# Kernel tuning notes

Hardware: AMD Instinct MI355X
Metric: run time of the kernel (lower is better)

Reference implementation:

```python
import jax, jax.numpy as jnp
import numpy as np

B, N, E = 8, 1024, 512
H, D = 8, 64
F = 2048


def setup_inputs() -> dict:
    key = jax.random.key(0)
    ks = jax.random.split(key, 12)
    s = lambda *sh: 1.0 / np.sqrt(sh[-1])
    inp = {
        "input1": jax.random.normal(ks[0], (B, N, E), dtype=jnp.float32),
        # projection weights stored as [in, out] (torch weight transposed)
        "Wq": jax.random.normal(ks[1], (E, H * D), dtype=jnp.float32) * s(E, E),
        "Wk": jax.random.normal(ks[2], (E, H * D), dtype=jnp.float32) * s(E, E),
        "Wv": jax.random.normal(ks[3], (E, H * D), dtype=jnp.float32) * s(E, E),
        "Wo": jax.random.normal(ks[4], (H * D, E), dtype=jnp.float32) * s(E, E),
        "bo": jnp.zeros((E,), dtype=jnp.float32),
        "g1": jnp.ones((E,), dtype=jnp.float32),
        "b1": jnp.zeros((E,), dtype=jnp.float32),
        "W1": jax.random.normal(ks[5], (E, F), dtype=jnp.float32) * s(E, E),
        "bf1": jnp.zeros((F,), dtype=jnp.float32),
        "W2": jax.random.normal(ks[6], (F, E), dtype=jnp.float32) * s(F, F),
        "bf2": jnp.zeros((E,), dtype=jnp.float32),
        "g2": jnp.ones((E,), dtype=jnp.float32),
        "b2": jnp.zeros((E,), dtype=jnp.float32),
    }
    return inp


def _layernorm(x, g, b, eps=1e-5):
    mu = jnp.mean(x, axis=-1, keepdims=True)
    var = jnp.var(x, axis=-1, keepdims=True)
    return (x - mu) * jax.lax.rsqrt(var + eps) * g + b


def reference(input1, Wq, Wk, Wv, Wo, bo, g1, b1, W1, bf1, W2, bf2, g2, b2):
    x = input1
    # QKV projections, split heads: [B, H, N, D]
    q = (x @ Wq).reshape(B, N, H, D).transpose(0, 2, 1, 3)
    k = (x @ Wk).reshape(B, N, H, D).transpose(0, 2, 1, 3)
    v = (x @ Wv).reshape(B, N, H, D).transpose(0, 2, 1, 3)
    # scaled dot-product attention (naive, materialized scores as in source)
    score = jnp.einsum("bhnd,bhmd->bhnm", q, k) / jnp.sqrt(jnp.float32(D))
    weights = jax.nn.softmax(score, axis=-1)
    out = jnp.einsum("bhnm,bhmd->bhnd", weights, v)
    out_concat = out.transpose(0, 2, 1, 3).reshape(B, N, H * D)
    mh = out_concat @ Wo + bo
    out1 = _layernorm(x + mh, g1, b1)
    ff = jax.nn.relu(out1 @ W1 + bf1) @ W2 + bf2
    out3 = _layernorm(out1 + ff, g2, b2)
    return (out3, 0)
```

## Files before the change

kernel.cpp:

```cpp
#include <hip/hip_runtime.h>
#include <cstdint>
#include <cstddef>

typedef _Float16 h8 __attribute__((ext_vector_type(8)));
typedef _Float16 h4 __attribute__((ext_vector_type(4)));
typedef __fp16   g2 __attribute__((ext_vector_type(2)));
typedef float    f32x4 __attribute__((ext_vector_type(4)));

constexpr int B_ = 8, N_ = 1024, E_ = 512, H_ = 8, D_ = 64, F_ = 2048;
constexpr int M_ = B_ * N_;
constexpr int HD_ = H_ * D_;

#define QSCALE2 0.18033688011112042f

#define GLOAD_LDS16(gp, lp)                                                        \
    __builtin_amdgcn_global_load_lds((const __attribute__((address_space(1))) void*)(gp), \
                                     (__attribute__((address_space(3))) void*)(lp), 16, 0, 0)

__device__ __forceinline__ float exp2_raw(float x) {
#if __has_builtin(__builtin_amdgcn_exp2f)
    return __builtin_amdgcn_exp2f(x);
#else
    float r;
    asm("v_exp_f32 %0, %1\n\ts_nop 0" : "=v"(r) : "v"(x));
    return r;
#endif
}

__global__ void __launch_bounds__(256) k_pre(
    const float* __restrict__ x, _Float16* __restrict__ xh,
    const float* __restrict__ Wq, const float* __restrict__ Wk,
    const float* __restrict__ Wv, const float* __restrict__ Wo,
    const float* __restrict__ W1, const float* __restrict__ W2,
    _Float16* __restrict__ oqkv, _Float16* __restrict__ oo,
    _Float16* __restrict__ o1, _Float16* __restrict__ o2) {
    if (blockIdx.z == 12) {
        int i = (blockIdx.x * 256 + threadIdx.x) * 16;
#pragma unroll
        for (int j = 0; j < 4; ++j) {
            float4 v = *(const float4*)(x + i + j * 4);
            h4 o = {(_Float16)v.x, (_Float16)v.y, (_Float16)v.z, (_Float16)v.w};
            *(h4*)(xh + i + j * 4) = o;
        }
        return;
    }
    if (blockIdx.x >= 256) return;
    const float* in;
    _Float16* out;
    int R, C, gt = blockIdx.x;
    switch (blockIdx.z) {
        case 0: in = Wq; out = oqkv;              R = 512;  C = 512;  break;
        case 1: in = Wk; out = oqkv + 512 * 512;  R = 512;  C = 512;  break;
        case 2: in = Wv; out = oqkv + 1024 * 512; R = 512;  C = 512;  break;
        case 3: in = Wo; out = oo;                R = 512;  C = 512;  break;
        default:
            if (blockIdx.z < 8) { in = W1; out = o1; R = 512;  C = 2048; gt += (blockIdx.z - 4) * 256; }
            else                { in = W2; out = o2; R = 2048; C = 512;  gt += (blockIdx.z - 8) * 256; }
    }
    const int ctiles = C >> 5;
    const int ty = gt / ctiles, tx = gt - ty * ctiles;
    const int r0 = ty * 32, c0 = tx * 32;
    __shared__ float lt[32][33];
    const int rr = threadIdx.x >> 3, cq = threadIdx.x & 7;
    float4 v = *(const float4*)&in[(size_t)(r0 + rr) * C + c0 + cq * 4];
    lt[rr][cq * 4 + 0] = v.x; lt[rr][cq * 4 + 1] = v.y;
    lt[rr][cq * 4 + 2] = v.z; lt[rr][cq * 4 + 3] = v.w;
    __syncthreads();
    h4 o = {(_Float16)lt[cq * 4 + 0][rr], (_Float16)lt[cq * 4 + 1][rr],
            (_Float16)lt[cq * 4 + 2][rr], (_Float16)lt[cq * 4 + 3][rr]};
    *(h4*)&out[(size_t)(c0 + rr) * R + r0 + cq * 4] = o;
}

template <int EPI>
__global__ void __launch_bounds__(256) k_gemm(
    const _Float16* __restrict__ A, const _Float16* __restrict__ Bt,
    int Mg, int Ng, int Kg,
    const float* __restrict__ bias,
    _Float16* __restrict__ outh,
    _Float16* __restrict__ qp, _Float16* __restrict__ kp, _Float16* __restrict__ vtp) {
    constexpr int BN = 128;
    constexpr int WN = BN / 2;
    constexpr int NI = WN / 16;
    __shared__ alignas(16) _Float16 lA[2][64 * 64];
    __shared__ alignas(16) _Float16 lB[2][BN * 64];

    const int tid = threadIdx.x;
    const int lane = tid & 63;
    const int wid = tid >> 6;
    const int wr = wid >> 1, wc = wid & 1;
    const int r16 = lane & 15, hseg = lane >> 4;

    const int bid = blockIdx.x;
    const int xcd = bid & 7;
    const int rem = bid >> 3;
    const int tx = rem >> 4, tyl = rem & 15;
    const int m0 = (xcd * 16 + tyl) * 64;
    const int n0 = tx * BN;

    auto STAGE = [&](int buf, int k0) {
#pragma unroll
        for (int i = 0; i < 2; ++i) {
            const int slot = i * 256 + tid, row = slot >> 3;
            const int cs = (slot & 7) ^ (row & 7);
            GLOAD_LDS16(A + (size_t)(m0 + row) * Kg + k0 + cs * 8, &lA[buf][slot * 8]);
        }
#pragma unroll
        for (int i = 0; i < BN / 32; ++i) {
            const int slot = i * 256 + tid, row = slot >> 3;
            const int cs = (slot & 7) ^ (row & 7);
            GLOAD_LDS16(Bt + (size_t)(n0 + row) * Kg + k0 + cs * 8, &lB[buf][slot * 8]);
        }
    };

    f32x4 acc[2][NI] = {};
    const int nt = Kg >> 6;

    STAGE(0, 0);
    __syncthreads();

    for (int t = 0; t < nt; ++t) {
        const int cur = t & 1;
        if (t + 1 < nt) STAGE(cur ^ 1, (t + 1) << 6);

#pragma unroll
        for (int kk = 0; kk < 2; ++kk) {
            h8 af[2], bf[NI];
#pragma unroll
            for (int mi = 0; mi < 2; ++mi) {
                const int row = wr * 32 + mi * 16 + r16;
                af[mi] = *(const h8*)&lA[cur][row * 64 + (((kk * 4 + hseg) ^ (row & 7)) * 8)];
            }
#pragma unroll
            for (int ni = 0; ni < NI; ++ni) {
                const int row = wc * WN + ni * 16 + r16;
                bf[ni] = *(const h8*)&lB[cur][row * 64 + (((kk * 4 + hseg) ^ (row & 7)) * 8)];
            }
#pragma unroll
            for (int mi = 0; mi < 2; ++mi)
#pragma unroll
                for (int ni = 0; ni < NI; ++ni)
                    acc[mi][ni] =
                        __builtin_amdgcn_mfma_f32_16x16x32_f16(af[mi], bf[ni], acc[mi][ni], 0, 0, 0);
        }
        __syncthreads();
    }

    if constexpr (EPI == 0) {
        if (n0 >= 1024) {
            _Float16* lC = &lA[0][0];
#pragma unroll
            for (int mi = 0; mi < 2; ++mi) {
                const int r0 = wr * 32 + mi * 16 + hseg * 4;
                const int s = r0 >> 3, ro = r0 & 7;
#pragma unroll
                for (int ni = 0; ni < NI; ++ni) {
                    const int c = wc * WN + ni * 16 + r16;
                    h4 pv = {(_Float16)acc[mi][ni][0], (_Float16)acc[mi][ni][1],
                             (_Float16)acc[mi][ni][2], (_Float16)acc[mi][ni][3]};
                    *(h4*)&lC[c * 64 + ((s ^ (c & 7)) << 3) + ro] = pv;
                }
            }
            __syncthreads();
            const int c = tid >> 1, half = tid & 1;
            const int b = m0 >> 10, nn0 = m0 & 1023;
            _Float16* gdst =
                vtp + ((size_t)(b * 512 + (n0 - 1024) + c)) * 1024 + nn0 + half * 32;
#pragma unroll
            for (int j = 0; j < 4; ++j) {
                const int s = half * 4 + j;
                h8 v = *(const h8*)&lC[c * 64 + ((s ^ (c & 7)) << 3)];
                *(h8*)&gdst[j * 8] = v;
            }
        } else {
#pragma unroll
            for (int mi = 0; mi < 2; ++mi)
#pragma unroll
                for (int ni = 0; ni < NI; ++ni)
#pragma unroll
                    for (int r = 0; r < 4; ++r) {
                        int row = m0 + wr * 32 + mi * 16 + hseg * 4 + r;
                        int col = n0 + wc * WN + ni * 16 + r16;
                        float v = acc[mi][ni][r];
                        int cc = col & 511;
                        int h = cc >> 6, d = cc & 63;
                        int b = row >> 10, nn = row & 1023;
                        if (col < 512)
                            qp[((b * 8 + h) * 1024 + nn) * 64 + d] = (_Float16)(v * QSCALE2);
                        else
                            kp[((b * 8 + h) * 1024 + nn) * 64 + d] = (_Float16)v;
                    }
        }
    } else {
#pragma unroll
        for (int mi = 0; mi < 2; ++mi)
#pragma unroll
            for (int ni = 0; ni < NI; ++ni)
#pragma unroll
                for (int r = 0; r < 4; ++r) {
                    int row = m0 + wr * 32 + mi * 16 + hseg * 4 + r;
                    int col = n0 + wc * WN + ni * 16 + r16;
                    float v = acc[mi][ni][r] + bias[col];
                    v = v > 0.f ? v : 0.f;
                    outh[(size_t)row * Ng + col] = (_Float16)v;
                }
    }
}

__global__ void __launch_bounds__(512) k_gemm64(
    const _Float16* __restrict__ A, const _Float16* __restrict__ Bt,
    int Ng, int Kg,
    const float* __restrict__ bias,
    const _Float16* __restrict__ resh, _Float16* __restrict__ outh) {
    __shared__ alignas(16) _Float16 lA[2][128 * 64];
    __shared__ alignas(16) _Float16 lB[2][64 * 64];

    const int tid = threadIdx.x;
    const int lane = tid & 63;
    const int wid = tid >> 6;
    const int wr = wid >> 1;
    const int wc = wid & 1;
    const int r16 = lane & 15, hseg = lane >> 4;

    const int bid = blockIdx.x;
    const int xcd = bid & 7;
    const int rem = bid >> 3;
    const int tx = rem >> 3, tyl = rem & 7;
    const int m0 = (xcd * 8 + tyl) * 128;
    const int n0 = tx * 64;

    auto STAGE = [&](int buf, int k0) {
#pragma unroll
        for (int i = 0; i < 2; ++i) {
            const int slot = i * 512 + tid, row = slot >> 3;
            const int cs = (slot & 7) ^ (row & 7);
            GLOAD_LDS16(A + (size_t)(m0 + row) * Kg + k0 + cs * 8, &lA[buf][slot * 8]);
        }
        {
            const int slot = tid, row = slot >> 3;
            const int cs = (slot & 7) ^ (row & 7);
            GLOAD_LDS16(Bt + (size_t)(n0 + row) * Kg + k0 + cs * 8, &lB[buf][slot * 8]);
        }
    };

    f32x4 acc[2][2] = {};
    const int nt = Kg >> 6;

    STAGE(0, 0);
    __syncthreads();

    for (int t = 0; t < nt; ++t) {
        const int cur = t & 1;
        if (t + 1 < nt) STAGE(cur ^ 1, (t + 1) << 6);

#pragma unroll
        for (int kk = 0; kk < 2; ++kk) {
            h8 af[2], bf[2];
#pragma unroll
            for (int mi = 0; mi < 2; ++mi) {
                const int row = wr * 32 + mi * 16 + r16;
                af[mi] = *(const h8*)&lA[cur][row * 64 + (((kk * 4 + hseg) ^ (row & 7)) * 8)];
            }
#pragma unroll
            for (int ni = 0; ni < 2; ++ni) {
                const int row = wc * 32 + ni * 16 + r16;
                bf[ni] = *(const h8*)&lB[cur][row * 64 + (((kk * 4 + hseg) ^ (row & 7)) * 8)];
            }
#pragma unroll
            for (int mi = 0; mi < 2; ++mi)
#pragma unroll
                for (int ni = 0; ni < 2; ++ni)
                    acc[mi][ni] =
                        __builtin_amdgcn_mfma_f32_16x16x32_f16(af[mi], bf[ni], acc[mi][ni], 0, 0, 0);
        }
        __syncthreads();
    }

#pragma unroll
    for (int mi = 0; mi < 2; ++mi)
#pragma unroll
        for (int ni = 0; ni < 2; ++ni)
#pragma unroll
            for (int r = 0; r < 4; ++r) {
                int row = m0 + wr * 32 + mi * 16 + hseg * 4 + r;
                int col = n0 + wc * 32 + ni * 16 + r16;
                float v = acc[mi][ni][r] + bias[col] + (float)resh[(size_t)row * Ng + col];
                outh[(size_t)row * Ng + col] = (_Float16)v;
            }
}

__global__ void __launch_bounds__(512) k_attn(const _Float16* __restrict__ q,
                                              const _Float16* __restrict__ k,
                                              const _Float16* __restrict__ vt,
                                              _Float16* __restrict__ attn) {
    __shared__ alignas(16) _Float16 lK[2][64 * 64];
    __shared__ alignas(16) _Float16 lV[2][64 * 64];
    __shared__ alignas(16) _Float16 lP[8][16 * 64];

    const int tid = threadIdx.x, lane = tid & 63, w = tid >> 6;
    const int bid = blockIdx.x;
    const int xcd = bid & 7, rem = bid >> 3;
    const int bh = xcd * 8 + (rem & 7);
    const int q0 = (rem >> 3) * 128;
    const int r16 = lane & 15, hseg = lane >> 4;
    const size_t base = (size_t)bh * N_ * D_;

    h8 qf0 = *(const h8*)&q[base + (size_t)(q0 + w * 16 + r16) * 64 + hseg * 8];
    h8 qf1 = *(const h8*)&q[base + (size_t)(q0 + w * 16 + r16) * 64 + 32 + hseg * 8];

    const int srow = tid >> 3;
    const int scsrc = (tid & 7) ^ (srow & 7);

    auto STAGE = [&](int buf, int kt) {
        GLOAD_LDS16(k + base + kt * 4096 + srow * 64 + scsrc * 8, &lK[buf][tid * 8]);
        GLOAD_LDS16(vt + base + (size_t)srow * N_ + kt * 64 + scsrc * 8, &lV[buf][tid * 8]);
    };

    float mrun = -1e30f, lrun = 0.f;
    f32x4 oacc[4] = {};

    const char* lKb = (const char*)&lK[0][0];
    const char* lVb = (const char*)&lV[0][0];
    char* lPb = (char*)&lP[0][0] + w * 2048;
    const int swz = r16 & 7;
    const int kb0 = r16 * 128 + ((hseg ^ swz) * 16);
    const int kb1 = r16 * 128 + (((4 + hseg) ^ swz) * 16);
    const int pswz = swz * 8;
    const int prd0 = r16 * 128 + (((hseg * 8) ^ pswz) * 2);
    const int prd1 = r16 * 128 + (((32 + hseg * 8) ^ pswz) * 2);
    const int pwr0 = r16 * 128 + (((0 + hseg * 4) ^ pswz) * 2);
    const int pwr1 = r16 * 128 + (((16 + hseg * 4) ^ pswz) * 2);
    const int pwr2 = r16 * 128 + (((32 + hseg * 4) ^ pswz) * 2);
    const int pwr3 = r16 * 128 + (((48 + hseg * 4) ^ pswz) * 2);

    auto TILE = [&](const int cur, const int kt) __attribute__((always_inline)) {
        if (kt + 1 < N_ / 64) STAGE(cur ^ 1, kt + 1);
        const int cOff = cur * 8192;

        float sv[4][4];
        __builtin_amdgcn_s_setprio(1);
#pragma unroll
        for (int t4 = 0; t4 < 4; ++t4) {
            f32x4 a = {};
            h8 kf0 = *(const h8*)(lKb + cOff + t4 * 2048 + kb0);
            a = __builtin_amdgcn_mfma_f32_16x16x32_f16(kf0, qf0, a, 0, 0, 0);
            h8 kf1 = *(const h8*)(lKb + cOff + t4 * 2048 + kb1);
            a = __builtin_amdgcn_mfma_f32_16x16x32_f16(kf1, qf1, a, 0, 0, 0);
#pragma unroll
            for (int r = 0; r < 4; ++r) sv[t4][r] = a[r];
        }
        __builtin_amdgcn_s_setprio(0);

        float m0a = fmaxf(fmaxf(sv[0][0], sv[0][1]), fmaxf(sv[0][2], sv[0][3]));
        float m1a = fmaxf(fmaxf(sv[1][0], sv[1][1]), fmaxf(sv[1][2], sv[1][3]));
        float m2a = fmaxf(fmaxf(sv[2][0], sv[2][1]), fmaxf(sv[2][2], sv[2][3]));
        float m3a = fmaxf(fmaxf(sv[3][0], sv[3][1]), fmaxf(sv[3][2], sv[3][3]));
        float mx = fmaxf(fmaxf(m0a, m1a), fmaxf(m2a, m3a));

        if (__any(mx > mrun + 8.f)) {
            mx = fmaxf(mx, __shfl_xor(mx, 16));
            mx = fmaxf(mx, __shfl_xor(mx, 32));
            float mnew = fmaxf(mrun, mx);
            float sc = exp2_raw(mrun - mnew);
            mrun = mnew;
            lrun *= sc;
#pragma unroll
            for (int r = 0; r < 4; ++r) {
                float scq = __shfl(sc, hseg * 4 + r);
#pragma unroll
                for (int nf = 0; nf < 4; ++nf) oacc[nf][r] *= scq;
            }
        }

        float p[4][4];
        float rsum = 0.f;
#pragma unroll
        for (int t4 = 0; t4 < 4; ++t4)
#pragma unroll
            for (int r = 0; r < 4; ++r) {
                p[t4][r] = exp2_raw(sv[t4][r] - mrun);
                rsum += p[t4][r];
            }
        lrun += rsum;

#pragma unroll
        for (int t4 = 0; t4 < 4; ++t4) {
            g2 a0 = __builtin_amdgcn_cvt_pkrtz(p[t4][0], p[t4][1]);
            g2 a1 = __builtin_amdgcn_cvt_pkrtz(p[t4][2], p[t4][3]);
            h4 pv = {(_Float16)a0[0], (_Float16)a0[1], (_Float16)a1[0], (_Float16)a1[1]};
            char* dst = lPb + (t4 == 0 ? pwr0 : t4 == 1 ? pwr1 : t4 == 2 ? pwr2 : pwr3);
            *(h4*)dst = pv;
        }
        asm volatile("s_waitcnt lgkmcnt(0)" ::: "memory");

        h8 pa0 = *(const h8*)(lPb + prd0);
        h8 pa1 = *(const h8*)(lPb + prd1);
        __builtin_amdgcn_s_setprio(1);
#pragma unroll
        for (int nf = 0; nf < 4; ++nf) {
            h8 vb0 = *(const h8*)(lVb + cOff + nf * 2048 + kb0);
            oacc[nf] = __builtin_amdgcn_mfma_f32_16x16x32_f16(pa0, vb0, oacc[nf], 0, 0, 0);
            h8 vb1 = *(const h8*)(lVb + cOff + nf * 2048 + kb1);
            oacc[nf] = __builtin_amdgcn_mfma_f32_16x16x32_f16(pa1, vb1, oacc[nf], 0, 0, 0);
        }
        __builtin_amdgcn_s_setprio(0);
        __syncthreads();
    };

    STAGE(0, 0);
    __syncthreads();

    for (int kt = 0; kt < N_ / 64; kt += 2) {
        TILE(0, kt);
        TILE(1, kt + 1);
    }

    lrun += __shfl_xor(lrun, 16);
    lrun += __shfl_xor(lrun, 32);

    float rlin = 1.f / lrun;
    int b = bh >> 3, h = bh & 7;
#pragma unroll
    for (int r = 0; r < 4; ++r) {
        float inv = __shfl(rlin, hseg * 4 + r);
        int row = b * 1024 + q0 + w * 16 + hseg * 4 + r;
#pragma unroll
        for (int nf = 0; nf < 4; ++nf) {
            int col = h * 64 + nf * 16 + r16;
            attn[(size_t)row * 512 + col] = (_Float16)(oacc[nf][r] * inv);
        }
    }
}

template <int OUTF32>
__global__ void __launch_bounds__(256) k_ln(const _Float16* __restrict__ x,
                                            const float* __restrict__ g,
                                            const float* __restrict__ b,
                                            float* __restrict__ outf,
                                            _Float16* __restrict__ outh,
                                            float* __restrict__ tail) {
    int row = blockIdx.x * 4 + (threadIdx.x >> 6);
    int lane = threadIdx.x & 63;
    h8 v = *(const h8*)(x + (size_t)row * 512 + lane * 8);
    float f[8];
    float s = 0.f, sq = 0.f;
#pragma unroll
    for (int j = 0; j < 8; ++j) {
        f[j] = (float)v[j];
        s += f[j];
        sq += f[j] * f[j];
    }
#pragma unroll
    for (int msk = 1; msk < 64; msk <<= 1) {
        s += __shfl_xor(s, msk);
        sq += __shfl_xor(sq, msk);
    }
    float mu = s * (1.f / 512.f);
    float var = sq * (1.f / 512.f) - mu * mu;
    float rstd = rsqrtf(var + 1e-5f);
    float4 ga = *(const float4*)(g + lane * 8);
    float4 gb = *(const float4*)(g + lane * 8 + 4);
    float4 ba = *(const float4*)(b + lane * 8);
    float4 bb = *(const float4*)(b + lane * 8 + 4);
    float o[8];
    o[0] = (f[0] - mu) * rstd * ga.x + ba.x;
    o[1] = (f[1] - mu) * rstd * ga.y + ba.y;
    o[2] = (f[2] - mu) * rstd * ga.z + ba.z;
    o[3] = (f[3] - mu) * rstd * ga.w + ba.w;
    o[4] = (f[4] - mu) * rstd * gb.x + bb.x;
    o[5] = (f[5] - mu) * rstd * gb.y + bb.y;
    o[6] = (f[6] - mu) * rstd * gb.z + bb.z;
    o[7] = (f[7] - mu) * rstd * gb.w + bb.w;
    if constexpr (OUTF32) {
        float* orow = outf + (size_t)row * 512 + lane * 8;
        *(float4*)(orow) = make_float4(o[0], o[1], o[2], o[3]);
        *(float4*)(orow + 4) = make_float4(o[4], o[5], o[6], o[7]);
        if (tail && blockIdx.x == 0 && threadIdx.x == 0) tail[0] = 0.f;
    } else {
        h8 oh = {(_Float16)o[0], (_Float16)o[1], (_Float16)o[2], (_Float16)o[3],
                 (_Float16)o[4], (_Float16)o[5], (_Float16)o[6], (_Float16)o[7]};
        *(h8*)(outh + (size_t)row * 512 + lane * 8) = oh;
    }
}

extern "C" void kernel_launch(void* const* d_in, const int* in_sizes, int n_in,
                              void* d_out, int out_size, void* d_ws, size_t ws_size,
                              hipStream_t stream) {
    const float* x   = (const float*)d_in[0];
    const float* Wq  = (const float*)d_in[1];
    const float* Wk  = (const float*)d_in[2];
    const float* Wv  = (const float*)d_in[3];
    const float* Wo  = (const float*)d_in[4];
    const float* bo  = (const float*)d_in[5];
    const float* g1  = (const float*)d_in[6];
    const float* b1  = (const float*)d_in[7];
    const float* W1  = (const float*)d_in[8];
    const float* bf1 = (const float*)d_in[9];
    const float* W2  = (const float*)d_in[10];
    const float* bf2 = (const float*)d_in[11];
    const float* g2  = (const float*)d_in[12];
    const float* b2  = (const float*)d_in[13];
    float* out = (float*)d_out;

    char* ws = (char*)d_ws;
    _Float16* xh    = (_Float16*)(ws + 0);
    _Float16* wqkvT = (_Float16*)(ws + 8388608);
    _Float16* woT   = (_Float16*)(ws + 9961472);
    _Float16* w1T   = (_Float16*)(ws + 10485760);
    _Float16* w2T   = (_Float16*)(ws + 12582912);
    _Float16* qb    = (_Float16*)(ws + 14680064);
    _Float16* kb    = (_Float16*)(ws + 23068672);
    _Float16* vtb   = (_Float16*)(ws + 31457280);
    _Float16* attnb = (_Float16*)(ws + 39845888);
    _Float16* h1h   = (_Float16*)(ws + 48234496);
    _Float16* out1h = xh;
    _Float16* ff    = qb;

    k_pre<<<dim3(1024, 1, 13), 256, 0, stream>>>(x, xh, Wq, Wk, Wv, Wo, W1, W2,
                                                 wqkvT, woT, w1T, w2T);

    k_gemm<0><<<dim3(1536), 256, 0, stream>>>(
        xh, wqkvT, M_, 1536, 512, nullptr, nullptr, qb, kb, vtb);

    k_attn<<<dim3(512), 512, 0, stream>>>(qb, kb, vtb, attnb);

    k_gemm64<<<dim3(512), 512, 0, stream>>>(attnb, woT, 512, 512, bo, xh, h1h);

    k_ln<0><<<dim3(M_ / 4), 256, 0, stream>>>(h1h, g1, b1, nullptr, out1h, nullptr);

    k_gemm<2><<<dim3(2048), 256, 0, stream>>>(
        out1h, w1T, M_, 2048, 512, bf1, ff, nullptr, nullptr, nullptr);

    k_gemm64<<<dim3(512), 512, 0, stream>>>(ff, w2T, 512, 2048, bf2, out1h, h1h);

    k_ln<1><<<dim3(M_ / 4), 256, 0, stream>>>(h1h, g2, b2, out, nullptr, out + (size_t)M_ * E_);
}
```

Measured before the change: 144.6 us.

## Triple-buffer GEMM LDS staging with vmcnt waits and one barrier per tile

Both GEMM kernels move from double-buffered LDS staging with two __syncthreads per K-step to a three-stage ring. Loads run two tiles ahead, and each iteration waits with a partial s_waitcnt vmcnt plus a single s_barrier. The K-tile count becomes a compile-time constant so the loop fully unrolls. This should hide more global-load latency and remove a barrier per iteration, at the cost of 50% more LDS per block and hand-tuned vmcnt counts that depend on how many loads each STAGE issues.

```diff
diff --git a/kernel.cpp b/kernel.cpp
--- a/kernel.cpp
+++ b/kernel.cpp
@@ -81,8 +81,9 @@
     constexpr int BN = 128;
     constexpr int WN = BN / 2;
     constexpr int NI = WN / 16;
-    __shared__ alignas(16) _Float16 lA[2][64 * 64];
-    __shared__ alignas(16) _Float16 lB[2][BN * 64];
+    constexpr int NT = 8;
+    __shared__ alignas(16) _Float16 lA[3][64 * 64];
+    __shared__ alignas(16) _Float16 lB[3][BN * 64];
 
     const int tid = threadIdx.x;
     const int lane = tid & 63;
@@ -113,27 +114,20 @@
     };
 
     f32x4 acc[2][NI] = {};
-    const int nt = Kg >> 6;
-
-    STAGE(0, 0);
-    __syncthreads();
-
-    for (int t = 0; t < nt; ++t) {
-        const int cur = t & 1;
-        if (t + 1 < nt) STAGE(cur ^ 1, (t + 1) << 6);
-
+
+    auto COMPUTE = [&](const int buf) __attribute__((always_inline)) {
 #pragma unroll
         for (int kk = 0; kk < 2; ++kk) {
             h8 af[2], bf[NI];
 #pragma unroll
             for (int mi = 0; mi < 2; ++mi) {
                 const int row = wr * 32 + mi * 16 + r16;
-                af[mi] = *(const h8*)&lA[cur][row * 64 + (((kk * 4 + hseg) ^ (row & 7)) * 8)];
+                af[mi] = *(const h8*)&lA[buf][row * 64 + (((kk * 4 + hseg) ^ (row & 7)) * 8)];
             }
 #pragma unroll
             for (int ni = 0; ni < NI; ++ni) {
                 const int row = wc * WN + ni * 16 + r16;
-                bf[ni] = *(const h8*)&lB[cur][row * 64 + (((kk * 4 + hseg) ^ (row & 7)) * 8)];
+                bf[ni] = *(const h8*)&lB[buf][row * 64 + (((kk * 4 + hseg) ^ (row & 7)) * 8)];
             }
 #pragma unroll
             for (int mi = 0; mi < 2; ++mi)
@@ -142,11 +136,22 @@
                     acc[mi][ni] =
                         __builtin_amdgcn_mfma_f32_16x16x32_f16(af[mi], bf[ni], acc[mi][ni], 0, 0, 0);
         }
-        __syncthreads();
+    };
+
+    STAGE(0, 0);
+    STAGE(1, 64);
+#pragma unroll
+    for (int t = 0; t < NT; ++t) {
+        if (t < NT - 1) asm volatile("s_waitcnt vmcnt(6)" ::: "memory");
+        else            asm volatile("s_waitcnt vmcnt(0)" ::: "memory");
+        __builtin_amdgcn_s_barrier();
+        if (t + 2 < NT) STAGE((t + 2) % 3, (t + 2) * 64);
+        COMPUTE(t % 3);
     }
 
     if constexpr (EPI == 0) {
         if (n0 >= 1024) {
+            __syncthreads();
             _Float16* lC = &lA[0][0];
 #pragma unroll
             for (int mi = 0; mi < 2; ++mi) {
@@ -206,13 +211,14 @@
     }
 }
 
+template <int NT>
 __global__ void __launch_bounds__(512) k_gemm64(
     const _Float16* __restrict__ A, const _Float16* __restrict__ Bt,
     int Ng, int Kg,
     const float* __restrict__ bias,
     const _Float16* __restrict__ resh, _Float16* __restrict__ outh) {
-    __shared__ alignas(16) _Float16 lA[2][128 * 64];
-    __shared__ alignas(16) _Float16 lB[2][64 * 64];
+    __shared__ alignas(16) _Float16 lA[3][128 * 64];
+    __shared__ alignas(16) _Float16 lB[3][64 * 64];
 
     const int tid = threadIdx.x;
     const int lane = tid & 63;
@@ -243,27 +249,20 @@
     };
 
     f32x4 acc[2][2] = {};
-    const int nt = Kg >> 6;
-
-    STAGE(0, 0);
-    __syncthreads();
-
-    for (int t = 0; t < nt; ++t) {
-        const int cur = t & 1;
-        if (t + 1 < nt) STAGE(cur ^ 1, (t + 1) << 6);
-
+
+    auto COMPUTE = [&](const int buf) __attribute__((always_inline)) {
 #pragma unroll
         for (int kk = 0; kk < 2; ++kk) {
             h8 af[2], bf[2];
 #pragma unroll
             for (int mi = 0; mi < 2; ++mi) {
                 const int row = wr * 32 + mi * 16 + r16;
-                af[mi] = *(const h8*)&lA[cur][row * 64 + (((kk * 4 + hseg) ^ (row & 7)) * 8)];
+                af[mi] = *(const h8*)&lA[buf][row * 64 + (((kk * 4 + hseg) ^ (row & 7)) * 8)];
             }
 #pragma unroll
             for (int ni = 0; ni < 2; ++ni) {
                 const int row = wc * 32 + ni * 16 + r16;
-                bf[ni] = *(const h8*)&lB[cur][row * 64 + (((kk * 4 + hseg) ^ (row & 7)) * 8)];
+                bf[ni] = *(const h8*)&lB[buf][row * 64 + (((kk * 4 + hseg) ^ (row & 7)) * 8)];
             }
 #pragma unroll
             for (int mi = 0; mi < 2; ++mi)
@@ -272,7 +271,17 @@
                     acc[mi][ni] =
                         __builtin_amdgcn_mfma_f32_16x16x32_f16(af[mi], bf[ni], acc[mi][ni], 0, 0, 0);
         }
-        __syncthreads();
+    };
+
+    STAGE(0, 0);
+    STAGE(1, 64);
+#pragma unroll
+    for (int t = 0; t < NT; ++t) {
+        if (t < NT - 1) asm volatile("s_waitcnt vmcnt(3)" ::: "memory");
+        else            asm volatile("s_waitcnt vmcnt(0)" ::: "memory");
+        __builtin_amdgcn_s_barrier();
+        if (t + 2 < NT) STAGE((t + 2) % 3, (t + 2) * 64);
+        COMPUTE(t % 3);
     }
 
 #pragma unroll
@@ -523,14 +532,14 @@
 
     k_attn<<<dim3(512), 512, 0, stream>>>(qb, kb, vtb, attnb);
 
-    k_gemm64<<<dim3(512), 512, 0, stream>>>(attnb, woT, 512, 512, bo, xh, h1h);
+    k_gemm64<8><<<dim3(512), 512, 0, stream>>>(attnb, woT, 512, 512, bo, xh, h1h);
 
     k_ln<0><<<dim3(M_ / 4), 256, 0, stream>>>(h1h, g1, b1, nullptr, out1h, nullptr);
 
     k_gemm<2><<<dim3(2048), 256, 0, stream>>>(
         out1h, w1T, M_, 2048, 512, bf1, ff, nullptr, nullptr, nullptr);
 
-    k_gemm64<<<dim3(512), 512, 0, stream>>>(ff, w2T, 512, 2048, bf2, out1h, h1h);
+    k_gemm64<32><<<dim3(512), 512, 0, stream>>>(ff, w2T, 512, 2048, bf2, out1h, h1h);
 
     k_ln<1><<<dim3(M_ / 4), 256, 0, stream>>>(h1h, g2, b2, out, nullptr, out + (size_t)M_ * E_);
 }
```

Measured after the change: 139.2 us (median of 3 runs). 1.04x faster.
